# Performance work log

Hardware: AMD Instinct MI355X
Metric: run time of the kernel (lower is better)

## Reference

```python
import jax, jax.numpy as jnp
import numpy as np
from jax import lax

VOCAB = 256
H = 1024
L = 2
B = 64
T = 512
RESIDUAL = True


def setup_inputs() -> dict:
    key = jax.random.key(0)
    ks = jax.random.split(key, 8)
    s_ih = 1.0 / np.sqrt(H)
    return {
        "X": jax.random.randint(ks[0], (B, T), 0, VOCAB),
        "embed": jax.random.normal(ks[1], (VOCAB, H), dtype=jnp.float32) * 0.02,
        "Wih": jax.random.normal(ks[2], (L, 4 * H, H), dtype=jnp.float32) * s_ih,
        "Whh": jax.random.normal(ks[3], (L, 4 * H, H), dtype=jnp.float32) * s_ih,
        "bih": jax.random.normal(ks[4], (L, 4 * H), dtype=jnp.float32) * s_ih,
        "bhh": jax.random.normal(ks[5], (L, 4 * H), dtype=jnp.float32) * s_ih,
        "Wout": jax.random.normal(ks[6], (VOCAB, H), dtype=jnp.float32) * s_ih,
        "bout": jax.random.normal(ks[7], (VOCAB,), dtype=jnp.float32) * s_ih,
    }


def reference(X, embed, Wih, Whh, bih, bhh, Wout, bout):
    # X: [B, T] int tokens. Original loops over t in [0, T-2]: feeds X[:, t]
    # through an L-layer (residual) LSTM one char at a time, accumulates
    # mean-over-batch cross entropy vs X[:, t+1], then divides by T.
    Bsz, Tlen = X.shape
    n_layers = Wih.shape[0]
    xs = embed[X[:, :-1]]          # [B, T-1, H] embedded inputs
    xs_t = jnp.swapaxes(xs, 0, 1)  # [T-1, B, H] time-major for scan

    def cell(carry, x_t):
        h, c = carry  # each [L, B, H]
        inp = x_t
        hs, cs = [], []
        for l in range(n_layers):
            # torch LSTM gate order: input, forget, cell(g), output
            gates = inp @ Wih[l].T + h[l] @ Whh[l].T + (bih[l] + bhh[l])
            i_g, f_g, g_g, o_g = jnp.split(gates, 4, axis=-1)
            c_l = jax.nn.sigmoid(f_g) * c[l] + jax.nn.sigmoid(i_g) * jnp.tanh(g_g)
            h_l = jax.nn.sigmoid(o_g) * jnp.tanh(c_l)
            hs.append(h_l)
            cs.append(c_l)
            inp = h_l + inp if RESIDUAL else h_l
        return (jnp.stack(hs), jnp.stack(cs)), inp

    init = (jnp.zeros((n_layers, Bsz, xs.shape[-1]), xs.dtype),
            jnp.zeros((n_layers, Bsz, xs.shape[-1]), xs.dtype))
    _, outs = lax.scan(cell, init, xs_t)       # [T-1, B, H]

    logits = outs @ Wout.T + bout              # [T-1, B, V]
    targets = X[:, 1:].T                        # [T-1, B]
    logp = jax.nn.log_softmax(logits, axis=-1)
    ce = -jnp.take_along_axis(logp, targets[..., None], axis=-1)[..., 0]  # [T-1, B]
    loss = ce.mean(axis=1).sum() / Tlen
    return loss
```

## Files before the change

kernel.cpp:

```cpp
#include <hip/hip_runtime.h>
#include <hip/hip_bf16.h>

typedef __hip_bfloat16 bf16;
typedef short v8s __attribute__((ext_vector_type(8)));
typedef float v4f __attribute__((ext_vector_type(4)));
typedef float v16f __attribute__((ext_vector_type(16)));
typedef unsigned long long u64;

static __device__ __forceinline__ float bf2f(bf16 x) { return __bfloat162float(x); }
static __device__ __forceinline__ unsigned short bfbits(float f) {
    bf16 t = __float2bfloat16(f);
    return *(unsigned short*)&t;
}
static __device__ __forceinline__ float fast_tanh(float x) {
    float e = __expf(-2.f * x);
    return (1.f - e) / (1.f + e);
}

__global__ __launch_bounds__(256) void k_zero(float* __restrict__ zbase, float* __restrict__ loss) {
    int idx = blockIdx.x * 256 + threadIdx.x;
    if (idx < 140288) zbase[idx] = 0.0f;
    if (idx == 0) loss[0] = 0.0f;
}

__global__ __launch_bounds__(256) void k_convert_w(const float* __restrict__ Wih,
                                                   const float* __restrict__ Whh,
                                                   bf16* __restrict__ Wb) {
    int idx = blockIdx.x * 256 + threadIdx.x;
    int k2 = idx & 2047;
    int ln = idx >> 11;
    float v = (k2 < 1024) ? Wih[ln * 1024 + k2] : Whh[ln * 1024 + (k2 - 1024)];
    Wb[idx] = __float2bfloat16(v);
}

__global__ __launch_bounds__(256) void k_convert_small(const float* __restrict__ Wout,
                                                       const float* __restrict__ bih,
                                                       const float* __restrict__ bhh,
                                                       bf16* __restrict__ Wob,
                                                       float* __restrict__ bsum) {
    int idx = blockIdx.x * 256 + threadIdx.x;
    if (idx < 262144) Wob[idx] = __float2bfloat16(Wout[idx]);
    int bidx = idx - 262144;
    if (bidx >= 0 && bidx < 8192) bsum[bidx] = bih[bidx] + bhh[bidx];
}

__global__ __launch_bounds__(256) void k_embed(const int* __restrict__ X,
                                               const float* __restrict__ embed,
                                               bf16* __restrict__ x0) {
    int bi = blockIdx.x;
    int kc = bi & 3;
    int tb = bi >> 2;
    int b  = tb & 63;
    int t  = tb >> 6;
    int k  = kc * 256 + threadIdx.x;
    int tok = X[b * 512 + t];
    x0[(long)tb * 1024 + k] = __float2bfloat16(embed[tok * 1024 + k]);
}

#define GLDI_C(dst, p, o) asm volatile("global_load_dwordx4 %0, %1, off offset:%2"         : "=v"(dst) : "v"(p), "i"(o))
#define GLDI_B(dst, p, o) asm volatile("global_load_dwordx4 %0, %1, off offset:%2 sc0 sc1" : "=v"(dst) : "v"(p), "i"(o))
#define MFMA(acc, a, w) asm volatile("v_mfma_f32_32x32x16_bf16 %0, %1, %2, %0" : "+v"(acc) : "v"(a), "a"(w))
#define VW(n)  asm volatile("s_waitcnt vmcnt(%0)" :: "i"(n))
#define VW0()  asm volatile("s_waitcnt vmcnt(0)")
#define ZACC(a) do { _Pragma("unroll") for (int r_ = 0; r_ < 16; ++r_) a[r_] = 0.f; } while(0)

#define ISSUE(GLD, c, B) do { \
    GLD(B[0], pA0, (c)*128 +  0); GLD(B[1], pA1, (c)*128 +  0); \
    GLD(B[2], pA0, (c)*128 + 32); GLD(B[3], pA1, (c)*128 + 32); \
    GLD(B[4], pA0, (c)*128 + 64); GLD(B[5], pA1, (c)*128 + 64); \
    GLD(B[6], pA0, (c)*128 + 96); GLD(B[7], pA1, (c)*128 + 96); } while(0)

#define CHUNK(c, B) do { _Pragma("unroll") for (int i_ = 0; i_ < 4; ++i_) { \
    MFMA(acc00, B[2*i_],   wa0[(c)*4+i_]); \
    MFMA(acc10, B[2*i_+1], wa0[(c)*4+i_]); \
    MFMA(acc01, B[2*i_],   wa1[(c)*4+i_]); \
    MFMA(acc11, B[2*i_+1], wa1[(c)*4+i_]); } } while(0)

#define PIPE(GLD) do { \
    ISSUE(GLD,0,bufa); ISSUE(GLD,1,bufb); ISSUE(GLD,2,bufc); ISSUE(GLD,3,bufd); \
    VW(24); CHUNK(0,bufa); ISSUE(GLD,4,bufa); \
    VW(24); CHUNK(1,bufb); ISSUE(GLD,5,bufb); \
    VW(24); CHUNK(2,bufc); ISSUE(GLD,6,bufc); \
    VW(24); CHUNK(3,bufd); ISSUE(GLD,7,bufd); \
    VW(24); CHUNK(4,bufa); \
    VW(16); CHUNK(5,bufb); \
    VW(8);  CHUNK(6,bufc); \
    VW(0);  CHUNK(7,bufd); } while(0)

#define WRGP(OP) do { _Pragma("unroll") for (int r_ = 0; r_ < 16; ++r_) { \
    const int grow_ = (r_&3) + ((r_>>2)<<3) + ((l>>5)<<2); \
    gp[q&1][grow_][l&31]          OP acc00[r_]; \
    gp[q&1][grow_][32+(l&31)]     OP acc01[r_]; \
    gp[q&1][32+grow_][l&31]       OP acc10[r_]; \
    gp[q&1][32+grow_][32+(l&31)]  OP acc11[r_]; } } while(0)

__global__ __launch_bounds__(256, 1) void k_lstm(bf16* __restrict__ x0all,
                                                 bf16* __restrict__ x1buf,
                                                 bf16* __restrict__ h0buf,
                                                 bf16* __restrict__ h1buf,
                                                 const bf16* __restrict__ Wb,
                                                 const float* __restrict__ bsum,
                                                 unsigned* bar) {
    __shared__ float gp[2][64][67];
    __shared__ float c_lds[64][17];
    __shared__ float b_lds[64];

    const int g     = blockIdx.x;
    const int layer = g >> 6;
    const int j     = g & 63;
    const int tid   = threadIdx.x;
    const int l     = tid & 63;
    const int q     = tid >> 6;

    unsigned* myline = bar + ((layer << 3) + (j & 7)) * 32;
    unsigned* rdline = bar + (16 + (j & 7)) * 32;

    if (tid < 64) b_lds[tid] = bsum[layer * 4096 + (tid >> 4) * 1024 + (j << 4) + (tid & 15)];
    for (int i = tid; i < 64 * 17; i += 256) ((float*)c_lds)[i] = 0.f;

    const int nl0 = l & 31, nl1 = 32 + (l & 31);
    const long N0 = (long)((nl0 >> 4) * 1024 + (j << 4) + (nl0 & 15));
    const long N1 = (long)((nl1 >> 4) * 1024 + (j << 4) + (nl1 & 15));
    const bf16* wp0 = Wb + (long)layer * 8388608 + N0 * 2048 + q * 512 + ((l >> 5) << 3);
    const bf16* wp1 = Wb + (long)layer * 8388608 + N1 * 2048 + q * 512 + ((l >> 5) << 3);
    v8s wa0[32], wa1[32];
#pragma unroll
    for (int kk = 0; kk < 32; ++kk) {
        wa0[kk] = *(const v8s*)(wp0 + kk * 16);
        asm volatile("" : "+a"(wa0[kk]));
        wa1[kk] = *(const v8s*)(wp1 + kk * 16);
        asm volatile("" : "+a"(wa1[kk]));
    }

    const int ab = tid >> 2;
    const int dq = tid & 3;
    const int off_ = ab * 1024 + (j << 4) + dq * 4;
    const bool prewave = (layer == 0) && (q < 2);
    const int li = l & 31;
    const bool lineused = (layer == 0) ? (li < 8 || (li >= 16 && li < 24))
                                       : (li < 16);

#pragma unroll 1
    for (int s = 0; s < 512; ++s) {
        const bool act = (layer == 0) ? (s < 511) : (s >= 1);
        const bf16* xop = x0all + (long)s * 65536;
        const bf16* x1p = x1buf + ((s + 1) & 1) * 65536;
        const bf16* h0p = h0buf + ((s + 1) & 1) * 65536;
        const bf16* h1p = h1buf + ((s + 1) & 1) * 65536;
        bf16* hdst  = (layer ? h1buf : h0buf) + (s & 1) * 65536;
        bf16* x1dst = x1buf + (s & 1) * 65536;
        bf16* res1  = x0all + (long)(s - 1) * 65536;

        const bf16* base = (layer == 0) ? ((q < 2) ? xop : h0p)
                                        : ((q < 2) ? x1p : h1p);
        const bf16* pA0 = base + ((q & 1) << 9) + (l & 31) * 1024 + ((l >> 5) << 3);
        const bf16* pA1 = pA0 + 32 * 1024;

        v16f acc00, acc01, acc10, acc11;
        v8s bufa[8], bufb[8], bufc[8], bufd[8];
        u64 xv = 0;

        if (act && layer == 0) xv = *(const u64*)(xop + off_);
        if (act && prewave) {
            ZACC(acc00); ZACC(acc01); ZACC(acc10); ZACC(acc11);
            PIPE(GLDI_C);
            WRGP(=);
        }
        if (s > 0 && q == 0) {
            const unsigned* lp = bar + li * 32;
            const unsigned req = lineused ? 8u * (unsigned)s : 0u;
            for (;;) {
                unsigned v;
                asm volatile("global_load_dword %0, %1, off sc0 sc1\n\t"
                             "s_waitcnt vmcnt(0)" : "=v"(v) : "v"(lp));
                if (__ballot(v >= req) == ~0ull) break;
            }
        }
        __syncthreads();
        if (act && !prewave) {
            if (layer == 1) {
                const bf16* xrp = x1p + off_;
                asm volatile("global_load_dwordx2 %0, %1, off sc0 sc1" : "=v"(xv) : "v"(xrp));
            }
            ZACC(acc00); ZACC(acc01); ZACC(acc10); ZACC(acc11);
            PIPE(GLDI_B);
            if (q < 2) WRGP(=);
        }
        __syncthreads();
        if (layer == 1 && tid == 0)
            __hip_atomic_fetch_add(rdline, 1u, __ATOMIC_RELAXED, __HIP_MEMORY_SCOPE_AGENT);
        if (act && q >= 2) WRGP(+=);
        __syncthreads();

        if (act) {
            float hv4[4];
#pragma unroll
            for (int i = 0; i < 4; ++i) {
                const int d = dq * 4 + i;
                const float gi = gp[0][ab][d]      + gp[1][ab][d]      + b_lds[d];
                const float gf = gp[0][ab][16 + d] + gp[1][ab][16 + d] + b_lds[16 + d];
                const float gg = gp[0][ab][32 + d] + gp[1][ab][32 + d] + b_lds[32 + d];
                const float go = gp[0][ab][48 + d] + gp[1][ab][48 + d] + b_lds[48 + d];
                const float si = 1.f / (1.f + __expf(-gi));
                const float sf = 1.f / (1.f + __expf(-gf));
                const float so = 1.f / (1.f + __expf(-go));
                const float tg = fast_tanh(gg);
                const float cn = sf * c_lds[ab][d] + si * tg;
                c_lds[ab][d] = cn;
                hv4[i] = so * fast_tanh(cn);
            }
            u64 hv64 = 0, rv64 = 0;
#pragma unroll
            for (int i = 0; i < 4; ++i) {
                const unsigned us = (unsigned)((xv >> (16 * i)) & 0xffffu);
                const float rv = hv4[i] + __uint_as_float(us << 16);
                hv64 |= (u64)bfbits(hv4[i]) << (16 * i);
                rv64 |= (u64)bfbits(rv) << (16 * i);
            }
            bf16* hp = hdst + off_;
            asm volatile("global_store_dwordx2 %0, %1, off sc0 sc1" :: "v"(hp), "v"(hv64) : "memory");
            bf16* rp = (layer == 0) ? (x1dst + off_) : (res1 + off_);
            asm volatile("global_store_dwordx2 %0, %1, off sc0 sc1" :: "v"(rp), "v"(rv64) : "memory");
        }
        VW0();
        __syncthreads();
        if (tid == 0)
            __hip_atomic_fetch_add(myline, 1u, __ATOMIC_RELAXED, __HIP_MEMORY_SCOPE_AGENT);
    }
}

__global__ __launch_bounds__(256) void k_final(const bf16* __restrict__ outAll,
                                               const bf16* __restrict__ Wob,
                                               const float* __restrict__ bout,
                                               const int* __restrict__ X,
                                               float* __restrict__ loss) {
    const int t    = blockIdx.x;
    const int tid  = threadIdx.x;
    const int lane = tid & 63;
    const int w    = tid >> 6;
    const int col  = lane & 15;
    const int oct  = lane >> 4;
    const bf16* arow = outAll + ((long)t * 64 + (w << 4) + col) * 1024 + (oct << 3);
    v4f acc[16];
#pragma unroll
    for (int nt = 0; nt < 16; ++nt) acc[nt] = (v4f){0.f, 0.f, 0.f, 0.f};
    for (int k0 = 0; k0 < 1024; k0 += 32) {
        v8s a = *(const v8s*)(arow + k0);
#pragma unroll
        for (int nt = 0; nt < 16; ++nt) {
            v8s bb = *(const v8s*)(Wob + ((nt << 4) + col) * 1024 + (oct << 3) + k0);
            acc[nt] = __builtin_amdgcn_mfma_f32_16x16x32_bf16(a, bb, acc[nt], 0, 0, 0);
        }
    }
#pragma unroll
    for (int nt = 0; nt < 16; ++nt) {
        const float bb = bout[(nt << 4) + col];
        acc[nt][0] += bb; acc[nt][1] += bb; acc[nt][2] += bb; acc[nt][3] += bb;
    }
    float ce_sum = 0.f;
#pragma unroll
    for (int r = 0; r < 4; ++r) {
        float mx = -3.4e38f;
#pragma unroll
        for (int nt = 0; nt < 16; ++nt) mx = fmaxf(mx, acc[nt][r]);
#pragma unroll
        for (int mm = 1; mm < 16; mm <<= 1) mx = fmaxf(mx, __shfl_xor(mx, mm, 64));
        float ss = 0.f;
#pragma unroll
        for (int nt = 0; nt < 16; ++nt) ss += __expf(acc[nt][r] - mx);
#pragma unroll
        for (int mm = 1; mm < 16; mm <<= 1) ss += __shfl_xor(ss, mm, 64);
        const int b   = (w << 4) + (oct << 2) + r;
        const int tok = X[b * 512 + t + 1];
        float lt = 0.f;
#pragma unroll
        for (int nt = 0; nt < 16; ++nt)
            if ((tok >> 4) == nt) lt = acc[nt][r];
        if ((tok & 15) == col)
            ce_sum += mx + __logf(ss) - lt;
    }
#pragma unroll
    for (int mm = 1; mm < 64; mm <<= 1) ce_sum += __shfl_xor(ce_sum, mm, 64);
    if (lane == 0) atomicAdd(loss, ce_sum * (1.0f / 32768.0f));
}

extern "C" void kernel_launch(void* const* d_in, const int* in_sizes, int n_in,
                              void* d_out, int out_size, void* d_ws, size_t ws_size,
                              hipStream_t stream) {
    const int*   X     = (const int*)  d_in[0];
    const float* embed = (const float*)d_in[1];
    const float* Wih   = (const float*)d_in[2];
    const float* Whh   = (const float*)d_in[3];
    const float* bih   = (const float*)d_in[4];
    const float* bhh   = (const float*)d_in[5];
    const float* Wout  = (const float*)d_in[6];
    const float* bout  = (const float*)d_in[7];
    float* loss = (float*)d_out;

    char* ws = (char*)d_ws;
    bf16*     x0all = (bf16*)(ws + 0);
    bf16*     Wb    = (bf16*)(ws + 66977792);
    bf16*     Wob   = (bf16*)(ws + 100532224);
    bf16*     x1buf = (bf16*)(ws + 101056512);
    bf16*     h0buf = (bf16*)(ws + 101318656);
    bf16*     h1buf = (bf16*)(ws + 101580800);
    float*    bsum  = (float*)(ws + 101842944);
    unsigned* bar   = (unsigned*)(ws + 101875712);
    float*    zbase = (float*)(ws + 101318656);

    if (ws_size < 101879808u) return;

    k_zero<<<548, 256, 0, stream>>>(zbase, loss);
    k_convert_w<<<65536, 256, 0, stream>>>(Wih, Whh, Wb);
    k_convert_small<<<1056, 256, 0, stream>>>(Wout, bih, bhh, Wob, bsum);
    k_embed<<<130816, 256, 0, stream>>>(X, embed, x0all);

    void* args[] = {&x0all, &x1buf, &h0buf, &h1buf, &Wb, &bsum, &bar};
    hipLaunchCooperativeKernel((void*)k_lstm, dim3(128), dim3(256), args, 0, stream);

    k_final<<<511, 256, 0, stream>>>(x0all, Wob, bout, X, loss);
}
```

Baseline: 6.024 ms.

## Triple-buffer residual x1 buffer, drop layer-1 read barrier, relax cache scope bits

The residual activation buffer x1 is now triple-buffered, which lets layer 0 run one step ahead without waiting on layer 1's read acknowledgement, so the extra rdline atomic counter is removed. The spin-wait is restructured: only 16 lanes poll a barrier line, and layer-0 lines 8-15 require one step less. Global loads and stores of shared state drop the sc0 bit and keep only sc1, which changes cache coherence scope to cut memory latency on the recurrent critical path. The risks are the correctness of the relaxed ordering and a slightly larger workspace.

```diff
diff --git a/kernel.cpp b/kernel.cpp
--- a/kernel.cpp
+++ b/kernel.cpp
@@ -57,8 +57,8 @@
     x0[(long)tb * 1024 + k] = __float2bfloat16(embed[tok * 1024 + k]);
 }
 
-#define GLDI_C(dst, p, o) asm volatile("global_load_dwordx4 %0, %1, off offset:%2"         : "=v"(dst) : "v"(p), "i"(o))
-#define GLDI_B(dst, p, o) asm volatile("global_load_dwordx4 %0, %1, off offset:%2 sc0 sc1" : "=v"(dst) : "v"(p), "i"(o))
+#define GLDI_C(dst, p, o) asm volatile("global_load_dwordx4 %0, %1, off offset:%2"     : "=v"(dst) : "v"(p), "i"(o))
+#define GLDI_B(dst, p, o) asm volatile("global_load_dwordx4 %0, %1, off offset:%2 sc1" : "=v"(dst) : "v"(p), "i"(o))
 #define MFMA(acc, a, w) asm volatile("v_mfma_f32_32x32x16_bf16 %0, %1, %2, %0" : "+v"(acc) : "v"(a), "a"(w))
 #define VW(n)  asm volatile("s_waitcnt vmcnt(%0)" :: "i"(n))
 #define VW0()  asm volatile("s_waitcnt vmcnt(0)")
@@ -113,7 +113,6 @@
     const int q     = tid >> 6;
 
     unsigned* myline = bar + ((layer << 3) + (j & 7)) * 32;
-    unsigned* rdline = bar + (16 + (j & 7)) * 32;
 
     if (tid < 64) b_lds[tid] = bsum[layer * 4096 + (tid >> 4) * 1024 + (j << 4) + (tid & 15)];
     for (int i = tid; i < 64 * 17; i += 256) ((float*)c_lds)[i] = 0.f;
@@ -136,19 +135,19 @@
     const int dq = tid & 3;
     const int off_ = ab * 1024 + (j << 4) + dq * 4;
     const bool prewave = (layer == 0) && (q < 2);
-    const int li = l & 31;
-    const bool lineused = (layer == 0) ? (li < 8 || (li >= 16 && li < 24))
-                                       : (li < 16);
+
+    int s3 = 0;
 
 #pragma unroll 1
     for (int s = 0; s < 512; ++s) {
         const bool act = (layer == 0) ? (s < 511) : (s >= 1);
+        const int s3p = (s3 == 0) ? 2 : s3 - 1;
         const bf16* xop = x0all + (long)s * 65536;
-        const bf16* x1p = x1buf + ((s + 1) & 1) * 65536;
+        const bf16* x1p = x1buf + s3p * 65536;
         const bf16* h0p = h0buf + ((s + 1) & 1) * 65536;
         const bf16* h1p = h1buf + ((s + 1) & 1) * 65536;
         bf16* hdst  = (layer ? h1buf : h0buf) + (s & 1) * 65536;
-        bf16* x1dst = x1buf + (s & 1) * 65536;
+        bf16* x1dst = x1buf + s3 * 65536;
         bf16* res1  = x0all + (long)(s - 1) * 65536;
 
         const bf16* base = (layer == 0) ? ((q < 2) ? xop : h0p)
@@ -167,12 +166,15 @@
             WRGP(=);
         }
         if (s > 0 && q == 0) {
-            const unsigned* lp = bar + li * 32;
-            const unsigned req = lineused ? 8u * (unsigned)s : 0u;
+            unsigned req = 0;
+            if (l < 16)
+                req = (layer == 0 && l >= 8) ? (8u * (unsigned)s - 8u) : (8u * (unsigned)s);
+            const unsigned* lp = bar + l * 32;
             for (;;) {
-                unsigned v;
-                asm volatile("global_load_dword %0, %1, off sc0 sc1\n\t"
-                             "s_waitcnt vmcnt(0)" : "=v"(v) : "v"(lp));
+                unsigned v = req;
+                if (l < 16)
+                    asm volatile("global_load_dword %0, %1, off sc1\n\t"
+                                 "s_waitcnt vmcnt(0)" : "=v"(v) : "v"(lp));
                 if (__ballot(v >= req) == ~0ull) break;
             }
         }
@@ -180,15 +182,13 @@
         if (act && !prewave) {
             if (layer == 1) {
                 const bf16* xrp = x1p + off_;
-                asm volatile("global_load_dwordx2 %0, %1, off sc0 sc1" : "=v"(xv) : "v"(xrp));
+                asm volatile("global_load_dwordx2 %0, %1, off sc1" : "=v"(xv) : "v"(xrp));
             }
             ZACC(acc00); ZACC(acc01); ZACC(acc10); ZACC(acc11);
             PIPE(GLDI_B);
             if (q < 2) WRGP(=);
         }
         __syncthreads();
-        if (layer == 1 && tid == 0)
-            __hip_atomic_fetch_add(rdline, 1u, __ATOMIC_RELAXED, __HIP_MEMORY_SCOPE_AGENT);
         if (act && q >= 2) WRGP(+=);
         __syncthreads();
 
@@ -218,14 +218,15 @@
                 rv64 |= (u64)bfbits(rv) << (16 * i);
             }
             bf16* hp = hdst + off_;
-            asm volatile("global_store_dwordx2 %0, %1, off sc0 sc1" :: "v"(hp), "v"(hv64) : "memory");
+            asm volatile("global_store_dwordx2 %0, %1, off sc1" :: "v"(hp), "v"(hv64) : "memory");
             bf16* rp = (layer == 0) ? (x1dst + off_) : (res1 + off_);
-            asm volatile("global_store_dwordx2 %0, %1, off sc0 sc1" :: "v"(rp), "v"(rv64) : "memory");
+            asm volatile("global_store_dwordx2 %0, %1, off sc1" :: "v"(rp), "v"(rv64) : "memory");
         }
         VW0();
         __syncthreads();
         if (tid == 0)
             __hip_atomic_fetch_add(myline, 1u, __ATOMIC_RELAXED, __HIP_MEMORY_SCOPE_AGENT);
+        s3 = (s3 == 2) ? 0 : s3 + 1;
     }
 }
 
@@ -302,13 +303,13 @@
     bf16*     Wb    = (bf16*)(ws + 66977792);
     bf16*     Wob   = (bf16*)(ws + 100532224);
     bf16*     x1buf = (bf16*)(ws + 101056512);
-    bf16*     h0buf = (bf16*)(ws + 101318656);
-    bf16*     h1buf = (bf16*)(ws + 101580800);
-    float*    bsum  = (float*)(ws + 101842944);
-    unsigned* bar   = (unsigned*)(ws + 101875712);
-    float*    zbase = (float*)(ws + 101318656);
-
-    if (ws_size < 101879808u) return;
+    bf16*     h0buf = (bf16*)(ws + 101449728);
+    bf16*     h1buf = (bf16*)(ws + 101711872);
+    float*    bsum  = (float*)(ws + 101974016);
+    unsigned* bar   = (unsigned*)(ws + 102006784);
+    float*    zbase = (float*)(ws + 101449728);
+
+    if (ws_size < 102010880u) return;
 
     k_zero<<<548, 256, 0, stream>>>(zbase, loss);
     k_convert_w<<<65536, 256, 0, stream>>>(Wih, Whh, Wb);
```

New measurement: 6.028 ms. No clear change (+0.1%).
